# Performance work log

Measured on AMD Instinct MI355X. Metric: run time of the kernel, lower is better.

Reference implementation:

```python
import jax, jax.numpy as jnp
import numpy as np

N, E, D_IN, D_OUT = 16384, 4096, 256, 256


def _leaky(v):
    return jnp.where(v > 0, v, 0.1 * v)


def setup_inputs() -> dict:
    key = jax.random.key(0)
    ks = jax.random.split(key, 8)
    x = jax.random.normal(ks[0], (N, D_IN), dtype=jnp.float32)
    # 0/1 incidence mask, float32 (as multiplied in the torch code)
    H_shape = jax.random.randint(ks[1], (N, E), 0, 2).astype(jnp.float32)
    w1 = jax.random.normal(ks[2], (D_IN, D_OUT), dtype=jnp.float32)
    w2 = jax.random.normal(ks[3], (D_OUT, D_OUT), dtype=jnp.float32)
    a1 = jax.random.normal(ks[4], (D_OUT, 1), dtype=jnp.float32)
    a21 = jax.random.normal(ks[5], (D_OUT, 1), dtype=jnp.float32)
    a22 = jax.random.normal(ks[6], (D_OUT, 1), dtype=jnp.float32)
    return {"x": x, "H_shape": H_shape, "w1": w1, "w2": w2,
            "a1": a1, "a21": a21, "a22": a22}


def reference(x, H_shape, w1, w2, a1, a21, a22):
    xw1 = x @ w1                                  # [N, D]
    # node->edge attention (masked softmax-like over nodes, axis -2)
    f = _leaky(xw1) @ a1                          # [N, 1]
    e = jnp.exp(jnp.tanh(f / 8) * 8) * H_shape    # [N, E]
    e = e / jnp.sum(e, axis=-2, keepdims=True)    # normalize over nodes
    # edge features
    f = _leaky(e.T @ xw1)                         # [E, D]
    # edge->node attention (masked normalize over edges, axis -1)
    b = (_leaky(f @ w2) @ a21).T + _leaky(xw1) @ a22  # [1,E] + [N,1] -> [N,E]
    b = jnp.exp(jnp.tanh(b / 8) * 8) * H_shape
    b = b / jnp.sum(b, axis=-1, keepdims=True)
    return _leaky(b @ f @ w2)                     # [N, D]
```

## Files before the change

kernel.cpp:

```cpp
#include <hip/hip_runtime.h>


typedef __attribute__((ext_vector_type(8))) short short8;
typedef __attribute__((ext_vector_type(4))) short short4v;
typedef __attribute__((ext_vector_type(4))) float f32x4;
typedef __attribute__((ext_vector_type(4))) int int4v;
typedef __attribute__((ext_vector_type(4))) unsigned int uint4v;

__device__ __forceinline__ float leakyf(float v) { return v > 0.f ? v : 0.1f * v; }
__device__ __forceinline__ float fastrcp(float x) { return __builtin_amdgcn_rcpf(x); }

__device__ __forceinline__ float satexpf(float t) {
    float u = fminf(fmaxf(t * 0.25f, -30.f), 30.f);
    float p = __expf(u);
    float th = (p - 1.f) * fastrcp(p + 1.f);
    return __expf(8.f * th);
}

__device__ __forceinline__ short f2b(float v) {
    unsigned int x = __float_as_uint(v);
    x += 0x7fffu + ((x >> 16) & 1u);
    return (short)(x >> 16);
}
__device__ __forceinline__ float b2f(short s) {
    return __uint_as_float(((unsigned int)(unsigned short)s) << 16);
}
__device__ __forceinline__ unsigned int bits4_to_bytes(unsigned int s) {
    return ((s & 0xFu) * 0x00204081u) & 0x01010101u;
}

__global__ __launch_bounds__(256) void transpose_split2(
        const float* __restrict__ s0, short* __restrict__ dh0, short* __restrict__ dl0,
        const float* __restrict__ s1, short* __restrict__ dh1, short* __restrict__ dl1) {
    const float* src = blockIdx.z ? s1 : s0;
    short* dh = blockIdx.z ? dh1 : dh0;
    short* dl = blockIdx.z ? dl1 : dl0;
    __shared__ float Ts[64][65];
    const int t = threadIdx.x;
    const long r0 = (long)blockIdx.x * 64;
    const long c0 = (long)blockIdx.y * 64;
    {
        const int row = t >> 2, cc = (t & 3) * 16;
        const float* p = src + (r0 + row) * 256 + c0 + cc;
#pragma unroll
        for (int i = 0; i < 4; ++i) {
            f32x4 v = *reinterpret_cast<const f32x4*>(p + i * 4);
#pragma unroll
            for (int k = 0; k < 4; ++k) Ts[row][cc + i * 4 + k] = v[k];
        }
    }
    __syncthreads();
    {
        const int cl = t >> 2, ch = (t & 3) * 16;
        short8 h0, h1, l0, l1;
#pragma unroll
        for (int i = 0; i < 8; ++i) {
            float v = Ts[ch + i][cl];
            short h = f2b(v);
            h0[i] = h; l0[i] = f2b(v - b2f(h));
        }
#pragma unroll
        for (int i = 0; i < 8; ++i) {
            float v = Ts[ch + 8 + i][cl];
            short h = f2b(v);
            h1[i] = h; l1[i] = f2b(v - b2f(h));
        }
        short* qh = dh + (c0 + cl) * 256 + r0 + ch;
        short* ql = dl + (c0 + cl) * 256 + r0 + ch;
        *reinterpret_cast<short8*>(qh) = h0;
        *reinterpret_cast<short8*>(qh + 8) = h1;
        *reinterpret_cast<short8*>(ql) = l0;
        *reinterpret_cast<short8*>(ql + 8) = l1;
    }
}

__global__ __launch_bounds__(256) void transposeH_pack(
        const float* __restrict__ H, unsigned int* __restrict__ Hbits,
        unsigned int* __restrict__ HbitsT, unsigned int* __restrict__ ddmax,
        float* __restrict__ cat) {
    __shared__ float Ts[64][65];
    const int t = threadIdx.x;
    const long r0 = (long)blockIdx.x * 64;
    const long c0 = (long)blockIdx.y * 64;
    if (blockIdx.x == 0 && blockIdx.y == 0) {
        if (t < 256) ddmax[t] = 0u;
        if (t < 32) ddmax[256 + t] = 0u;
#pragma unroll
        for (int i = 0; i < 16; ++i) cat[t * 16 + i] = 0.f;
    }
    {
        const int row = t >> 2, cc = (t & 3) * 16;
        const float* p = H + (r0 + row) * 4096L + c0 + cc;
#pragma unroll
        for (int i = 0; i < 4; ++i) {
            f32x4 v = *reinterpret_cast<const f32x4*>(p + i * 4);
#pragma unroll
            for (int k = 0; k < 4; ++k) Ts[row][cc + i * 4 + k] = v[k];
        }
    }
    __syncthreads();
    if (t < 128) {
        const int nl = t >> 1, w = t & 1;
        unsigned int u = 0;
#pragma unroll
        for (int b = 0; b < 32; ++b)
            u |= (Ts[nl][w * 32 + b] != 0.f ? 1u : 0u) << b;
        Hbits[(r0 + nl) * 128 + (c0 >> 5) + w] = u;
    } else {
        const int t2 = t - 128;
        const int jl = t2 >> 1, w = t2 & 1;
        unsigned int u = 0;
#pragma unroll
        for (int b = 0; b < 32; ++b)
            u |= (Ts[w * 32 + b][jl] != 0.f ? 1u : 0u) << b;
        HbitsT[(c0 + jl) * 512 + (r0 >> 5) + w] = u;
    }
}

__global__ __launch_bounds__(256) void gemm_xw1(
        const float* __restrict__ A, const short* __restrict__ Bh,
        const short* __restrict__ Bl, float* __restrict__ C) {
    __shared__ short Ash[128][72];
    __shared__ short Asl[128][72];
    __shared__ short Bsh[64][72];
    __shared__ short Bsl[64][72];
    const int t = threadIdx.x;
    const int wid = t >> 6, lane = t & 63;
    const int wm = wid & 1, wn = wid >> 1;
    const int quad = lane >> 4, l15 = lane & 15;
    const long m0 = (long)blockIdx.x * 128;
    const long n0 = (long)blockIdx.y * 64;
    f32x4 acc[4][2];
#pragma unroll
    for (int i = 0; i < 4; ++i)
#pragma unroll
        for (int j = 0; j < 2; ++j)
#pragma unroll
            for (int r = 0; r < 4; ++r) acc[i][j][r] = 0.f;

    for (int kb = 0; kb < 256; kb += 64) {
#pragma unroll
        for (int it = 0; it < 4; ++it) {
            const int cid = t + it * 256;
            const int row = cid >> 3, c8 = (cid & 7) * 8;
            const float* ap = A + (m0 + row) * 256 + kb + c8;
            f32x4 v0 = *reinterpret_cast<const f32x4*>(ap);
            f32x4 v1 = *reinterpret_cast<const f32x4*>(ap + 4);
            short8 hi, lo;
#pragma unroll
            for (int k = 0; k < 4; ++k) {
                short h0 = f2b(v0[k]); hi[k] = h0; lo[k] = f2b(v0[k] - b2f(h0));
                short h1 = f2b(v1[k]); hi[4 + k] = h1; lo[4 + k] = f2b(v1[k] - b2f(h1));
            }
            *reinterpret_cast<short8*>(&Ash[row][c8]) = hi;
            *reinterpret_cast<short8*>(&Asl[row][c8]) = lo;
        }
#pragma unroll
        for (int it = 0; it < 2; ++it) {
            const int cid = t + it * 256;
            const int row = cid >> 3, c8 = (cid & 7) * 8;
            *reinterpret_cast<short8*>(&Bsh[row][c8]) =
                *reinterpret_cast<const short8*>(Bh + (n0 + row) * 256 + kb + c8);
            *reinterpret_cast<short8*>(&Bsl[row][c8]) =
                *reinterpret_cast<const short8*>(Bl + (n0 + row) * 256 + kb + c8);
        }
        __syncthreads();
#pragma unroll
        for (int ks = 0; ks < 2; ++ks) {
            short8 ah[4], al[4], bh[2], bl[2];
#pragma unroll
            for (int i = 0; i < 4; ++i) {
                ah[i] = *reinterpret_cast<const short8*>(&Ash[wm * 64 + i * 16 + l15][ks * 32 + quad * 8]);
                al[i] = *reinterpret_cast<const short8*>(&Asl[wm * 64 + i * 16 + l15][ks * 32 + quad * 8]);
            }
#pragma unroll
            for (int j = 0; j < 2; ++j) {
                bh[j] = *reinterpret_cast<const short8*>(&Bsh[wn * 32 + j * 16 + l15][ks * 32 + quad * 8]);
                bl[j] = *reinterpret_cast<const short8*>(&Bsl[wn * 32 + j * 16 + l15][ks * 32 + quad * 8]);
            }
#pragma unroll
            for (int i = 0; i < 4; ++i)
#pragma unroll
                for (int j = 0; j < 2; ++j) {
                    acc[i][j] = __builtin_amdgcn_mfma_f32_16x16x32_bf16(ah[i], bh[j], acc[i][j], 0, 0, 0);
                    acc[i][j] = __builtin_amdgcn_mfma_f32_16x16x32_bf16(ah[i], bl[j], acc[i][j], 0, 0, 0);
                    acc[i][j] = __builtin_amdgcn_mfma_f32_16x16x32_bf16(al[i], bh[j], acc[i][j], 0, 0, 0);
                }
        }
        __syncthreads();
    }
#pragma unroll
    for (int i = 0; i < 4; ++i) {
        const long grow = m0 + wm * 64 + i * 16 + quad * 4;
#pragma unroll
        for (int j = 0; j < 2; ++j) {
            const long gcol = n0 + wn * 32 + j * 16 + l15;
#pragma unroll
            for (int r = 0; r < 4; ++r)
                C[(grow + r) * 256 + gcol] = acc[i][j][r];
        }
    }
}

__global__ __launch_bounds__(256) void node_stats1(
        const float* __restrict__ xw1, const float* __restrict__ a1,
        const float* __restrict__ a22, float* __restrict__ g_out,
        float* __restrict__ dn, unsigned int* __restrict__ ddmax) {
    __shared__ float Mx[4][260];
    const int t = threadIdx.x;
    const int n0 = blockIdx.x * 64;
    const int r = t >> 2, q = t & 3;
    const long n = n0 + r;
    const float* xp = xw1 + n * 256 + q * 64;
    float vals[64];
    float facc = 0.f, dacc = 0.f;
#pragma unroll
    for (int i = 0; i < 16; ++i) {
        f32x4 v  = *reinterpret_cast<const f32x4*>(xp + i * 4);
        f32x4 b1 = *reinterpret_cast<const f32x4*>(a1 + q * 64 + i * 4);
        f32x4 b2 = *reinterpret_cast<const f32x4*>(a22 + q * 64 + i * 4);
#pragma unroll
        for (int k = 0; k < 4; ++k) {
            float lv = leakyf(v[k]);
            facc += lv * b1[k];
            dacc += lv * b2[k];
            vals[i * 4 + k] = v[k];
        }
    }
    facc += __shfl_xor(facc, 1); facc += __shfl_xor(facc, 2);
    dacc += __shfl_xor(dacc, 1); dacc += __shfl_xor(dacc, 2);
    const float g = satexpf(facc);
    if (q == 0) { dn[n] = dacc; g_out[n] = g; }
    float lm[64];
#pragma unroll
    for (int i = 0; i < 64; ++i) lm[i] = fabsf(vals[i] * g);
#pragma unroll
    for (int m = 4; m < 64; m <<= 1)
#pragma unroll
        for (int i = 0; i < 64; ++i) lm[i] = fmaxf(lm[i], __shfl_xor(lm[i], m));
    float gm = g;
#pragma unroll
    for (int m = 1; m < 64; m <<= 1) gm = fmaxf(gm, __shfl_xor(gm, m));
    const int wv = t >> 6, lane = t & 63;
    if (lane < 4) {
#pragma unroll
        for (int i = 0; i < 64; ++i) Mx[wv][lane * 64 + i] = lm[i];
    }
    if (lane == 0) Mx[wv][256] = gm;
    __syncthreads();
    if (t < 256) {
        float m = fmaxf(fmaxf(Mx[0][t], Mx[1][t]), fmaxf(Mx[2][t], Mx[3][t]));
        atomicMax(&ddmax[t], __float_as_uint(m));
    }
    if (t == 0) {
        float m = fmaxf(fmaxf(Mx[0][256], Mx[1][256]), fmaxf(Mx[2][256], Mx[3][256]));
        atomicMax(&ddmax[256], __float_as_uint(m));
    }
}

__global__ __launch_bounds__(256) void quantize_y(
        const float* __restrict__ xw1, const float* __restrict__ g_in,
        const unsigned int* __restrict__ ddmax, char* __restrict__ yQ) {
    __shared__ unsigned int Qh[257][16];
    __shared__ unsigned int Ql[257][16];
    const int t = threadIdx.x;
    const int n0 = blockIdx.x * 64;
    const int dd0 = (t >> 4) * 16;
    const int w = t & 15;
    const int r4 = w * 4;
    float s[16];
#pragma unroll
    for (int i = 0; i < 16; ++i)
        s[i] = 32512.f / __uint_as_float(ddmax[dd0 + i]);
    const float sg = 32512.f / __uint_as_float(ddmax[256]);
    unsigned int bh[16], bl[16];
#pragma unroll
    for (int i = 0; i < 16; ++i) { bh[i] = 0u; bl[i] = 0u; }
    unsigned int gh = 0u, gl = 0u;
#pragma unroll
    for (int rr = 0; rr < 4; ++rr) {
        const long n = n0 + r4 + rr;
        const float gg = g_in[n];
        const float* xp = xw1 + n * 256 + dd0;
#pragma unroll
        for (int c = 0; c < 4; ++c) {
            f32x4 v = *reinterpret_cast<const f32x4*>(xp + c * 4);
#pragma unroll
            for (int k = 0; k < 4; ++k) {
                const int i = c * 4 + k;
                int qv = __float2int_rn(v[k] * gg * s[i]);
                qv = max(-32639, min(32639, qv));
                const int qh = (qv + 128) >> 8;
                const int ql = qv - (qh << 8);
                bh[i] |= ((unsigned int)(qh & 255)) << (8 * rr);
                bl[i] |= ((unsigned int)(ql & 255)) << (8 * rr);
            }
        }
        if (t < 16) {
            int qv = __float2int_rn(gg * sg);
            qv = max(-32639, min(32639, qv));
            const int qh = (qv + 128) >> 8;
            const int ql = qv - (qh << 8);
            gh |= ((unsigned int)(qh & 255)) << (8 * rr);
            gl |= ((unsigned int)(ql & 255)) << (8 * rr);
        }
    }
#pragma unroll
    for (int i = 0; i < 16; ++i) { Qh[dd0 + i][w] = bh[i]; Ql[dd0 + i][w] = bl[i]; }
    if (t < 16) { Qh[256][t] = gh; Ql[256][t] = gl; }
    __syncthreads();
#pragma unroll
    for (int it = 0; it < 2; ++it) {
        const int dd = it * 256 + t;
        if (dd < 288) {
#pragma unroll
            for (int s2 = 0; s2 < 4; ++s2) {
                uint4v vh, vl;
                if (dd < 257) {
                    vh = *reinterpret_cast<const uint4v*>(&Qh[dd][s2 * 4]);
                    vl = *reinterpret_cast<const uint4v*>(&Ql[dd][s2 * 4]);
                } else {
#pragma unroll
                    for (int k = 0; k < 4; ++k) { vh[k] = 0u; vl[k] = 0u; }
                }
                *reinterpret_cast<uint4v*>(yQ + (long)dd * 16384 + n0 + s2 * 16) = vh;
                *reinterpret_cast<uint4v*>(yQ + (long)(288 + dd) * 16384 + n0 + s2 * 16) = vl;
            }
        }
    }
}

__global__ __launch_bounds__(256) void gemm_c1_bits(
        const unsigned int* __restrict__ HbitsT, const char* __restrict__ Bb,
        float* __restrict__ Cp) {
    __shared__ char Bsh[48][144];
    __shared__ char Bsl[48][144];
    const int t = threadIdx.x;
    const int wid = t >> 6, lane = t & 63;
    const int quad = lane >> 4, l15 = lane & 15;
    const long m0 = (long)blockIdx.x * 256;
    const long n0 = (long)blockIdx.y * 48;
    const long k0 = (long)blockIdx.z * 2048;
    float* Cz = Cp + (long)blockIdx.z * (4096L * 288);
    const unsigned int* bp[4];
#pragma unroll
    for (int i = 0; i < 4; ++i)
        bp[i] = HbitsT + (m0 + wid * 64 + i * 16 + l15) * 512 + (k0 >> 5);
    int4v acch[4][3], accl[4][3];
#pragma unroll
    for (int i = 0; i < 4; ++i)
#pragma unroll
        for (int j = 0; j < 3; ++j)
#pragma unroll
            for (int r = 0; r < 4; ++r) { acch[i][j][r] = 0; accl[i][j][r] = 0; }

    for (int kb = 0; kb < 2048; kb += 128) {
        uint4v bv[4];
#pragma unroll
        for (int i = 0; i < 4; ++i)
            bv[i] = *reinterpret_cast<const uint4v*>(bp[i] + (kb >> 5));
#pragma unroll
        for (int it = 0; it < 3; ++it) {
            const int cid = t + it * 256;
            const int idx = (cid < 384) ? cid : cid - 384;
            const int row = idx >> 3, seg = (idx & 7) * 16;
            char* dst = (cid >= 384) ? &Bsl[row][seg] : &Bsh[row][seg];
            const long srow = (cid >= 384) ? (288 + n0 + row) : (n0 + row);
            *reinterpret_cast<uint4v*>(dst) =
                *reinterpret_cast<const uint4v*>(Bb + srow * 16384 + k0 + kb + seg);
        }
        __syncthreads();
#pragma unroll
        for (int ks = 0; ks < 2; ++ks) {
            int4v af[4], bh[3], bl[3];
#pragma unroll
            for (int i = 0; i < 4; ++i) {
                const unsigned int u =
                    bv[i][ks * 2 + (quad >> 1)] >> ((quad & 1) * 16);
                uint4v e;
#pragma unroll
                for (int k = 0; k < 4; ++k) e[k] = bits4_to_bytes(u >> (4 * k));
                af[i] = __builtin_bit_cast(int4v, e);
            }
#pragma unroll
            for (int j = 0; j < 3; ++j) {
                bh[j] = *reinterpret_cast<const int4v*>(&Bsh[j * 16 + l15][ks * 64 + quad * 16]);
                bl[j] = *reinterpret_cast<const int4v*>(&Bsl[j * 16 + l15][ks * 64 + quad * 16]);
            }
#pragma unroll
            for (int i = 0; i < 4; ++i)
#pragma unroll
                for (int j = 0; j < 3; ++j) {
                    acch[i][j] = __builtin_amdgcn_mfma_i32_16x16x64_i8(af[i], bh[j], acch[i][j], 0, 0, 0);
                    accl[i][j] = __builtin_amdgcn_mfma_i32_16x16x64_i8(af[i], bl[j], accl[i][j], 0, 0, 0);
                }
        }
        __syncthreads();
    }
#pragma unroll
    for (int i = 0; i < 4; ++i) {
        const long grow = m0 + wid * 64 + i * 16 + quad * 4;
#pragma unroll
        for (int j = 0; j < 3; ++j) {
            const long gcol = n0 + j * 16 + l15;
#pragma unroll
            for (int r = 0; r < 4; ++r)
                Cz[(grow + r) * 288 + gcol] =
                    256.f * (float)acch[i][j][r] + (float)accl[i][j][r];
        }
    }
}

__global__ __launch_bounds__(256) void reduce_C1(
        const float* __restrict__ C1p, const unsigned int* __restrict__ ddmax,
        float* __restrict__ C1) {
    const int i = blockIdx.x * 256 + threadIdx.x;
    const int dd = i % 288;
    float s = 0.f;
#pragma unroll
    for (int z = 0; z < 8; ++z) s += C1p[(long)z * 4096 * 288 + i];
    C1[i] = s * (__uint_as_float(ddmax[dd]) * (1.f / 32512.f));
}

__global__ __launch_bounds__(256) void gemm_G(
        const float* __restrict__ C1, const short* __restrict__ w2Th,
        const short* __restrict__ w2Tl, const float* __restrict__ a21,
        short* __restrict__ GT, float* __restrict__ cat) {
    __shared__ short Ash[64][72];
    __shared__ short Asl[64][72];
    __shared__ short Bsh[64][72];
    __shared__ short Bsl[64][72];
    __shared__ float Gs[64][65];
    const int t = threadIdx.x;
    const int wid = t >> 6, lane = t & 63;
    const int wm = wid & 1, wn = wid >> 1;
    const int quad = lane >> 4, l15 = lane & 15;
    const long j0 = (long)blockIdx.x * 64;
    const long d0 = (long)blockIdx.y * 64;
    f32x4 acc[2][2];
#pragma unroll
    for (int i = 0; i < 2; ++i)
#pragma unroll
        for (int j = 0; j < 2; ++j)
#pragma unroll
            for (int r = 0; r < 4; ++r) acc[i][j][r] = 0.f;

    for (int kb = 0; kb < 256; kb += 64) {
#pragma unroll
        for (int it = 0; it < 2; ++it) {
            const int cid = t + it * 256;
            const int row = cid >> 3, c8 = (cid & 7) * 8;
            const float rd = fastrcp(C1[(j0 + row) * 288 + 256]);
            const float* ap = C1 + (j0 + row) * 288 + kb + c8;
            f32x4 v0 = *reinterpret_cast<const f32x4*>(ap);
            f32x4 v1 = *reinterpret_cast<const f32x4*>(ap + 4);
            short8 hi, lo;
#pragma unroll
            for (int k = 0; k < 4; ++k) {
                float f0 = leakyf(v0[k] * rd);
                float f1 = leakyf(v1[k] * rd);
                short h0 = f2b(f0); hi[k] = h0; lo[k] = f2b(f0 - b2f(h0));
                short h1 = f2b(f1); hi[4 + k] = h1; lo[4 + k] = f2b(f1 - b2f(h1));
            }
            *reinterpret_cast<short8*>(&Ash[row][c8]) = hi;
            *reinterpret_cast<short8*>(&Asl[row][c8]) = lo;
            *reinterpret_cast<short8*>(&Bsh[row][c8]) =
                *reinterpret_cast<const short8*>(w2Th + (d0 + row) * 256 + kb + c8);
            *reinterpret_cast<short8*>(&Bsl[row][c8]) =
                *reinterpret_cast<const short8*>(w2Tl + (d0 + row) * 256 + kb + c8);
        }
        __syncthreads();
#pragma unroll
        for (int ks = 0; ks < 2; ++ks) {
            short8 ah[2], al[2], bh[2], bl[2];
#pragma unroll
            for (int i = 0; i < 2; ++i) {
                ah[i] = *reinterpret_cast<const short8*>(&Ash[wm * 32 + i * 16 + l15][ks * 32 + quad * 8]);
                al[i] = *reinterpret_cast<const short8*>(&Asl[wm * 32 + i * 16 + l15][ks * 32 + quad * 8]);
            }
#pragma unroll
            for (int j = 0; j < 2; ++j) {
                bh[j] = *reinterpret_cast<const short8*>(&Bsh[wn * 32 + j * 16 + l15][ks * 32 + quad * 8]);
                bl[j] = *reinterpret_cast<const short8*>(&Bsl[wn * 32 + j * 16 + l15][ks * 32 + quad * 8]);
            }
#pragma unroll
            for (int i = 0; i < 2; ++i)
#pragma unroll
                for (int j = 0; j < 2; ++j) {
                    acc[i][j] = __builtin_amdgcn_mfma_f32_16x16x32_bf16(ah[i], bh[j], acc[i][j], 0, 0, 0);
                    acc[i][j] = __builtin_amdgcn_mfma_f32_16x16x32_bf16(ah[i], bl[j], acc[i][j], 0, 0, 0);
                    acc[i][j] = __builtin_amdgcn_mfma_f32_16x16x32_bf16(al[i], bh[j], acc[i][j], 0, 0, 0);
                }
        }
        __syncthreads();
    }
#pragma unroll
    for (int i = 0; i < 2; ++i)
#pragma unroll
        for (int j = 0; j < 2; ++j)
#pragma unroll
            for (int r = 0; r < 4; ++r)
                Gs[wm * 32 + i * 16 + quad * 4 + r][wn * 32 + j * 16 + l15] = acc[i][j][r];
    __syncthreads();
    {
        const int jl = t >> 2, q = t & 3;
        float cp = 0.f;
#pragma unroll
        for (int i = 0; i < 16; ++i) {
            const int d = q * 16 + i;
            cp += leakyf(Gs[jl][d]) * a21[d0 + d];
        }
        cp += __shfl_xor(cp, 1); cp += __shfl_xor(cp, 2);
        if (q == 0) atomicAdd(&cat[j0 + jl], cp);
    }
    {
        const int dl = t >> 2, q = t & 3;
        short8 pk0, pk1;
#pragma unroll
        for (int i = 0; i < 8; ++i) pk0[i] = f2b(Gs[q * 16 + i][dl]);
#pragma unroll
        for (int i = 0; i < 8; ++i) pk1[i] = f2b(Gs[q * 16 + 8 + i][dl]);
        short* gp = GT + (d0 + dl) * 4096 + j0 + q * 16;
        *reinterpret_cast<short8*>(gp) = pk0;
        *reinterpret_cast<short8*>(gp + 8) = pk1;
    }
}

__global__ __launch_bounds__(512, 4) void fused_out_split(
        const unsigned int* __restrict__ Hbits, const float* __restrict__ cat,
        const float* __restrict__ dn, const short* __restrict__ GT,
        float* __restrict__ outP, float* __restrict__ rsP) {
    __shared__ short As[64][72];
    __shared__ short Bs[256][72];
    __shared__ float rsS[64][8];
    const int t = threadIdx.x;
    const int wid = t >> 6, lane = t & 63;
    const int wm = wid >> 2, wn = wid & 3;
    const int quad = lane >> 4, l15 = lane & 15;
    const long m0 = (long)blockIdx.x * 64;
    const int z = blockIdx.y;
    const int kbase = z * 1024;
    const int r = t & 63, c8 = t >> 6;
    const float drow = dn[m0 + r];
    const int bo = (c8 & 3) * 8;

    f32x4 acc[2][4];
#pragma unroll
    for (int i = 0; i < 2; ++i)
#pragma unroll
        for (int j = 0; j < 4; ++j)
#pragma unroll
            for (int x = 0; x < 4; ++x) acc[i][j][x] = 0.f;
    float racc = 0.f;

    for (int kk = 0; kk < 1024; kk += 64) {
        const int kb = kbase + kk;
#pragma unroll
        for (int it = 0; it < 4; ++it) {
            const int cid = t + it * 512;
            const int row = cid >> 3, cc = (cid & 7) * 8;
            *reinterpret_cast<short8*>(&Bs[row][cc]) =
                *reinterpret_cast<const short8*>(GT + row * 4096 + kb + cc);
        }
        {
            const unsigned int w = Hbits[(m0 + r) * 128 + (kb >> 5) + (c8 >> 2)];
            f32x4 cv0 = *reinterpret_cast<const f32x4*>(cat + kb + c8 * 8);
            f32x4 cv1 = *reinterpret_cast<const f32x4*>(cat + kb + c8 * 8 + 4);
            short8 pk;
#pragma unroll
            for (int k = 0; k < 8; ++k) {
                const float cvk = (k < 4) ? cv0[k & 3] : cv1[k & 3];
                const float s = ((w >> (bo + k)) & 1u) ? satexpf(cvk + drow) : 0.f;
                const short sb = f2b(s);
                pk[k] = sb;
                racc += b2f(sb);
            }
            *reinterpret_cast<short8*>(&As[r][c8 * 8]) = pk;
        }
        __syncthreads();
#pragma unroll
        for (int ks = 0; ks < 2; ++ks) {
            short8 af[2], bf[4];
#pragma unroll
            for (int i = 0; i < 2; ++i)
                af[i] = *reinterpret_cast<const short8*>(
                        &As[wm * 32 + i * 16 + l15][ks * 32 + quad * 8]);
#pragma unroll
            for (int j = 0; j < 4; ++j)
                bf[j] = *reinterpret_cast<const short8*>(
                        &Bs[wn * 64 + j * 16 + l15][ks * 32 + quad * 8]);
#pragma unroll
            for (int i = 0; i < 2; ++i)
#pragma unroll
                for (int j = 0; j < 4; ++j)
                    acc[i][j] = __builtin_amdgcn_mfma_f32_16x16x32_bf16(
                            af[i], bf[j], acc[i][j], 0, 0, 0);
        }
        __syncthreads();
    }
    rsS[r][c8] = racc;
    __syncthreads();
    if (t < 64) {
        float s = 0.f;
#pragma unroll
        for (int i = 0; i < 8; ++i) s += rsS[t][i];
        rsP[z * 16384 + m0 + t] = s;
    }
    float* op = outP + (long)z * (16384L * 256);
#pragma unroll
    for (int i = 0; i < 2; ++i) {
#pragma unroll
        for (int j = 0; j < 4; ++j) {
            const long gcol = wn * 64 + j * 16 + l15;
#pragma unroll
            for (int x = 0; x < 4; ++x) {
                const long grow = m0 + wm * 32 + i * 16 + quad * 4 + x;
                op[grow * 256 + gcol] = acc[i][j][x];
            }
        }
    }
}

__global__ __launch_bounds__(256) void combine_out(
        const float* __restrict__ outP, const float* __restrict__ rsP,
        float* __restrict__ out) {
    const long i = ((long)blockIdx.x * 256 + threadIdx.x) * 4;
    const long n = i >> 8;
    f32x4 s = *reinterpret_cast<const f32x4*>(outP + i);
#pragma unroll
    for (int z = 1; z < 4; ++z) {
        f32x4 v = *reinterpret_cast<const f32x4*>(outP + (long)z * (16384L * 256) + i);
#pragma unroll
        for (int k = 0; k < 4; ++k) s[k] += v[k];
    }
    const float rinv = fastrcp(rsP[n] + rsP[16384 + n] + rsP[32768 + n] + rsP[49152 + n]);
    f32x4 o;
#pragma unroll
    for (int k = 0; k < 4; ++k) o[k] = leakyf(s[k] * rinv);
    *reinterpret_cast<f32x4*>(out + i) = o;
}

extern "C" void kernel_launch(void* const* d_in, const int* in_sizes, int n_in,
                              void* d_out, int out_size, void* d_ws, size_t ws_size,
                              hipStream_t stream) {
    const float* x   = (const float*)d_in[0];
    const float* H   = (const float*)d_in[1];
    const float* w1  = (const float*)d_in[2];
    const float* w2  = (const float*)d_in[3];
    const float* a1  = (const float*)d_in[4];
    const float* a21 = (const float*)d_in[5];
    const float* a22 = (const float*)d_in[6];
    float* out = (float*)d_out;
    char* ws = (char*)d_ws;

    float* xw1   = (float*)(ws + 0);
    float* C1p   = (float*)(ws + 0);
    char*  yQ    = (char*)(ws + 67108864);
    float* dn    = (float*)(ws + 76546048);
    float* g     = (float*)(ws + 76611584);
    unsigned int* ddmax = (unsigned int*)(ws + 76677120);
    short* w1Th  = (short*)(ws + 76681216);
    short* w1Tl  = (short*)(ws + 76812288);
    short* w2Th  = (short*)(ws + 76943360);
    short* w2Tl  = (short*)(ws + 77074432);
    float* C1    = (float*)(ws + 77205504);
    short* GT    = (short*)(ws + 81924096);
    float* cat   = (float*)(ws + 84021248);
    unsigned int* Hbits  = (unsigned int*)(ws + 84037632);
    unsigned int* HbitsT = (unsigned int*)(ws + 92426240);
    float* outP  = (float*)(ws + 134217728);
    float* rsP   = (float*)(ws + 201326592);

    transpose_split2<<<dim3(4, 4, 2), 256, 0, stream>>>(
            w1, w1Th, w1Tl, w2, w2Th, w2Tl);
    transposeH_pack<<<dim3(256, 64), 256, 0, stream>>>(H, Hbits, HbitsT, ddmax, cat);

    gemm_xw1<<<dim3(128, 4), 256, 0, stream>>>(x, w1Th, w1Tl, xw1);
    node_stats1<<<dim3(256), 256, 0, stream>>>(xw1, a1, a22, g, dn, ddmax);
    quantize_y<<<dim3(256), 256, 0, stream>>>(xw1, g, ddmax, yQ);

    gemm_c1_bits<<<dim3(16, 6, 8), 256, 0, stream>>>(HbitsT, yQ, C1p);
    reduce_C1<<<dim3(4608), 256, 0, stream>>>(C1p, ddmax, C1);

    gemm_G<<<dim3(64, 4), 256, 0, stream>>>(C1, w2Th, w2Tl, a21, GT, cat);

    fused_out_split<<<dim3(256, 4), 512, 0, stream>>>(Hbits, cat, dn, GT, outP, rsP);
    combine_out<<<dim3(4096), 256, 0, stream>>>(outP, rsP, out);
}
```

Baseline: 610.6 us.

## Register-prefetch next K tile in bit-GEMM and attention GEMM kernels

Both main GEMM loops now load the next K tile from global memory into registers before running the current tile's MFMAs. The second kernel also computes the next tile's masked saturating-exp weights after the MFMAs. This hides global-load latency and the transcendental work behind matrix math with a single LDS buffer. The cost is higher register pressure, which may lower occupancy.

New measurement: 598.9 us. No clear change (-1.9%).

```diff
diff --git a/kernel.cpp b/kernel.cpp
--- a/kernel.cpp
+++ b/kernel.cpp
@@ -346,6 +346,17 @@
 #pragma unroll
     for (int i = 0; i < 4; ++i)
         bp[i] = HbitsT + (m0 + wid * 64 + i * 16 + l15) * 512 + (k0 >> 5);
+    char* dstp[3];
+    long sbase[3];
+#pragma unroll
+    for (int it = 0; it < 3; ++it) {
+        const int cid = t + it * 256;
+        const int idx = (cid < 384) ? cid : cid - 384;
+        const int row = idx >> 3, seg = (idx & 7) * 16;
+        dstp[it] = (cid >= 384) ? &Bsl[row][seg] : &Bsh[row][seg];
+        const long srow = (cid >= 384) ? (288 + n0 + row) : (n0 + row);
+        sbase[it] = srow * 16384 + k0 + seg;
+    }
     int4v acch[4][3], accl[4][3];
 #pragma unroll
     for (int i = 0; i < 4; ++i)
@@ -354,22 +365,29 @@
 #pragma unroll
             for (int r = 0; r < 4; ++r) { acch[i][j][r] = 0; accl[i][j][r] = 0; }
 
+    uint4v bv[4], sv[3];
+#pragma unroll
+    for (int i = 0; i < 4; ++i)
+        bv[i] = *reinterpret_cast<const uint4v*>(bp[i]);
+#pragma unroll
+    for (int it = 0; it < 3; ++it)
+        sv[it] = *reinterpret_cast<const uint4v*>(Bb + sbase[it]);
+
     for (int kb = 0; kb < 2048; kb += 128) {
-        uint4v bv[4];
-#pragma unroll
-        for (int i = 0; i < 4; ++i)
-            bv[i] = *reinterpret_cast<const uint4v*>(bp[i] + (kb >> 5));
-#pragma unroll
-        for (int it = 0; it < 3; ++it) {
-            const int cid = t + it * 256;
-            const int idx = (cid < 384) ? cid : cid - 384;
-            const int row = idx >> 3, seg = (idx & 7) * 16;
-            char* dst = (cid >= 384) ? &Bsl[row][seg] : &Bsh[row][seg];
-            const long srow = (cid >= 384) ? (288 + n0 + row) : (n0 + row);
-            *reinterpret_cast<uint4v*>(dst) =
-                *reinterpret_cast<const uint4v*>(Bb + srow * 16384 + k0 + kb + seg);
-        }
+#pragma unroll
+        for (int it = 0; it < 3; ++it)
+            *reinterpret_cast<uint4v*>(dstp[it]) = sv[it];
         __syncthreads();
+        const bool pf = (kb < 1920);
+        uint4v bvn[4], svn[3];
+        if (pf) {
+#pragma unroll
+            for (int i = 0; i < 4; ++i)
+                bvn[i] = *reinterpret_cast<const uint4v*>(bp[i] + ((kb + 128) >> 5));
+#pragma unroll
+            for (int it = 0; it < 3; ++it)
+                svn[it] = *reinterpret_cast<const uint4v*>(Bb + sbase[it] + kb + 128);
+        }
 #pragma unroll
         for (int ks = 0; ks < 2; ++ks) {
             int4v af[4], bh[3], bl[3];
@@ -396,6 +414,12 @@
                 }
         }
         __syncthreads();
+        if (pf) {
+#pragma unroll
+            for (int i = 0; i < 4; ++i) bv[i] = bvn[i];
+#pragma unroll
+            for (int it = 0; it < 3; ++it) sv[it] = svn[it];
+        }
     }
 #pragma unroll
     for (int i = 0; i < 4; ++i) {
@@ -553,31 +577,55 @@
             for (int x = 0; x < 4; ++x) acc[i][j][x] = 0.f;
     float racc = 0.f;
 
-    for (int kk = 0; kk < 1024; kk += 64) {
-        const int kb = kbase + kk;
+    short8 gv[4];
+    short8 pkc;
+    {
+        const int kb = kbase;
 #pragma unroll
         for (int it = 0; it < 4; ++it) {
             const int cid = t + it * 512;
             const int row = cid >> 3, cc = (cid & 7) * 8;
-            *reinterpret_cast<short8*>(&Bs[row][cc]) =
-                *reinterpret_cast<const short8*>(GT + row * 4096 + kb + cc);
-        }
-        {
-            const unsigned int w = Hbits[(m0 + r) * 128 + (kb >> 5) + (c8 >> 2)];
-            f32x4 cv0 = *reinterpret_cast<const f32x4*>(cat + kb + c8 * 8);
-            f32x4 cv1 = *reinterpret_cast<const f32x4*>(cat + kb + c8 * 8 + 4);
-            short8 pk;
-#pragma unroll
-            for (int k = 0; k < 8; ++k) {
-                const float cvk = (k < 4) ? cv0[k & 3] : cv1[k & 3];
-                const float s = ((w >> (bo + k)) & 1u) ? satexpf(cvk + drow) : 0.f;
-                const short sb = f2b(s);
-                pk[k] = sb;
-                racc += b2f(sb);
-            }
-            *reinterpret_cast<short8*>(&As[r][c8 * 8]) = pk;
-        }
+            gv[it] = *reinterpret_cast<const short8*>(GT + row * 4096 + kb + cc);
+        }
+        const unsigned int w = Hbits[(m0 + r) * 128 + (kb >> 5) + (c8 >> 2)];
+        const f32x4 cv0 = *reinterpret_cast<const f32x4*>(cat + kb + c8 * 8);
+        const f32x4 cv1 = *reinterpret_cast<const f32x4*>(cat + kb + c8 * 8 + 4);
+#pragma unroll
+        for (int k = 0; k < 8; ++k) {
+            const float cvk = (k < 4) ? cv0[k & 3] : cv1[k & 3];
+            const float s = ((w >> (bo + k)) & 1u) ? satexpf(cvk + drow) : 0.f;
+            const short sb = f2b(s);
+            pkc[k] = sb;
+            racc += b2f(sb);
+        }
+    }
+
+    for (int kk = 0; kk < 1024; kk += 64) {
+#pragma unroll
+        for (int it = 0; it < 4; ++it) {
+            const int cid = t + it * 512;
+            const int row = cid >> 3, cc = (cid & 7) * 8;
+            *reinterpret_cast<short8*>(&Bs[row][cc]) = gv[it];
+        }
+        *reinterpret_cast<short8*>(&As[r][c8 * 8]) = pkc;
         __syncthreads();
+
+        const bool pf = (kk < 960);
+        unsigned int hw = 0u;
+        f32x4 cn0{}, cn1{};
+        if (pf) {
+            const int kn = kbase + kk + 64;
+#pragma unroll
+            for (int it = 0; it < 4; ++it) {
+                const int cid = t + it * 512;
+                const int row = cid >> 3, cc = (cid & 7) * 8;
+                gv[it] = *reinterpret_cast<const short8*>(GT + row * 4096 + kn + cc);
+            }
+            hw = Hbits[(m0 + r) * 128 + (kn >> 5) + (c8 >> 2)];
+            cn0 = *reinterpret_cast<const f32x4*>(cat + kn + c8 * 8);
+            cn1 = *reinterpret_cast<const f32x4*>(cat + kn + c8 * 8 + 4);
+        }
+
 #pragma unroll
         for (int ks = 0; ks < 2; ++ks) {
             short8 af[2], bf[4];
@@ -595,6 +643,17 @@
                 for (int j = 0; j < 4; ++j)
                     acc[i][j] = __builtin_amdgcn_mfma_f32_16x16x32_bf16(
                             af[i], bf[j], acc[i][j], 0, 0, 0);
+        }
+
+        if (pf) {
+#pragma unroll
+            for (int k = 0; k < 8; ++k) {
+                const float cvk = (k < 4) ? cn0[k & 3] : cn1[k & 3];
+                const float s = ((hw >> (bo + k)) & 1u) ? satexpf(cvk + drow) : 0.f;
+                const short sb = f2b(s);
+                pkc[k] = sb;
+                racc += b2f(sb);
+            }
         }
         __syncthreads();
     }
```
